# Kernel optimization log

Measured on AMD Instinct MI355X. Metric: run time of the kernel, lower is better.

Reference implementation:

```python
import jax, jax.numpy as jnp
import numpy as np

N = 100000   # nodes
E = 1600000  # directed edges
BN_EPS = 1e-5


def setup_inputs() -> dict:
    key = jax.random.key(0)
    ks = jax.random.split(key, 16)
    x = jax.random.normal(ks[0], (N, 24), dtype=jnp.float32)
    edge_index = jax.random.randint(ks[1], (2, E), 0, N, dtype=jnp.int32)

    def glorot(k, fan_in, fan_out):
        s = jnp.sqrt(6.0 / (fan_in + fan_out)).astype(jnp.float32)
        return jax.random.uniform(k, (fan_in, fan_out), jnp.float32, -s, s)

    return {
        "x": x, "edge_index": edge_index,
        "W1": glorot(ks[2], 24, 128),  "b1": jnp.zeros((128,), jnp.float32),
        "g1": jnp.ones((128,), jnp.float32), "be1": jnp.zeros((128,), jnp.float32),
        "W2": glorot(ks[3], 128, 128), "b2": jnp.zeros((128,), jnp.float32),
        "g2": jnp.ones((128,), jnp.float32), "be2": jnp.zeros((128,), jnp.float32),
        "W3": glorot(ks[4], 128, 64),  "b3": jnp.zeros((64,), jnp.float32),
        "g3": jnp.ones((64,), jnp.float32), "be3": jnp.zeros((64,), jnp.float32),
        "W4": glorot(ks[5], 64, 2),    "b4": jnp.zeros((2,), jnp.float32),
    }


def _gcn_norm(edge_index, n):
    # add self loops, compute D^{-1/2}(A+I)D^{-1/2} edge weights (PyG gcn_norm)
    loop = jnp.arange(n, dtype=edge_index.dtype)
    src = jnp.concatenate([edge_index[0], loop])
    dst = jnp.concatenate([edge_index[1], loop])
    deg = jax.ops.segment_sum(jnp.ones_like(src, dtype=jnp.float32), dst, num_segments=n)
    dinv = jnp.where(deg > 0, jax.lax.rsqrt(deg), 0.0)
    norm = dinv[src] * dinv[dst]  # [E+N]
    return src, dst, norm


def _gcn_conv(x, W, b, src, dst, norm, n):
    h = x @ W                                # [N, F_out] GEMM first (PyG order)
    msg = h[src] * norm[:, None]             # gather + edge scale
    agg = jax.ops.segment_sum(msg, dst, num_segments=n)  # scatter-add
    return agg + b


def _bn(x, gamma, beta):
    # BatchNorm1d, training-mode statistics (biased variance), dropout omitted (eval)
    mean = jnp.mean(x, axis=0)
    var = jnp.var(x, axis=0)
    return (x - mean) * jax.lax.rsqrt(var + BN_EPS) * gamma + beta


def reference(x, edge_index, W1, b1, g1, be1, W2, b2, g2, be2,
              W3, b3, g3, be3, W4, b4):
    n = x.shape[0]
    src, dst, norm = _gcn_norm(edge_index, n)
    h = _bn(jax.nn.relu(_gcn_conv(x, W1, b1, src, dst, norm, n)), g1, be1)
    h = _bn(jax.nn.relu(_gcn_conv(h, W2, b2, src, dst, norm, n)), g2, be2)
    h = _bn(jax.nn.relu(_gcn_conv(h, W3, b3, src, dst, norm, n)), g3, be3)
    out = _gcn_conv(h, W4, b4, src, dst, norm, n)
    return jax.nn.log_softmax(out, axis=1)
```

## Files before the change

### kernel.cpp

```cpp
#include <hip/hip_runtime.h>
#include <hip/hip_fp16.h>

#define BN_EPS 1e-5f

__global__ void k_zero_i(int* __restrict__ p, int n) {
    int i = blockIdx.x * blockDim.x + threadIdx.x;
    if (i < n) p[i] = 0;
}

__global__ void k_count(const int* __restrict__ dst, int* __restrict__ cnt, int E) {
    int e = blockIdx.x * blockDim.x + threadIdx.x;
    if (e < E) atomicAdd(&cnt[dst[e]], 1);
}

__global__ void k_dinv(const int* __restrict__ cnt, float* __restrict__ dinv, int n) {
    int i = blockIdx.x * blockDim.x + threadIdx.x;
    if (i < n) dinv[i] = rsqrtf((float)(cnt[i] + 1));
}

__global__ void k_scan1(const int* __restrict__ cnt, int* __restrict__ rs,
                        int* __restrict__ bsum, int n) {
    __shared__ int sh[1024];
    const int t = threadIdx.x;
    const int gid = blockIdx.x * 1024 + t;
    int v = (gid < n) ? cnt[gid] : 0;
    sh[t] = v;
    __syncthreads();
    for (int off = 1; off < 1024; off <<= 1) {
        int u = (t >= off) ? sh[t - off] : 0;
        __syncthreads();
        sh[t] += u;
        __syncthreads();
    }
    if (gid < n) rs[gid] = sh[t] - v;
    if (t == 1023) bsum[blockIdx.x] = sh[1023];
}

__global__ void k_scan2(int* __restrict__ bsum, int nb) {
    __shared__ int sh[1024];
    const int t = threadIdx.x;
    int v = (t < nb) ? bsum[t] : 0;
    sh[t] = v;
    __syncthreads();
    for (int off = 1; off < 1024; off <<= 1) {
        int u = (t >= off) ? sh[t - off] : 0;
        __syncthreads();
        sh[t] += u;
        __syncthreads();
    }
    if (t < nb) bsum[t] = sh[t] - v;
}

__global__ void k_scan3(int* __restrict__ rs, int* __restrict__ cur,
                        const int* __restrict__ bsum, int n) {
    int i = blockIdx.x * blockDim.x + threadIdx.x;
    if (i < n) {
        int v = rs[i] + bsum[i >> 10];
        rs[i] = v;
        cur[i] = v;
    }
}

__global__ void k_fillx(const int* __restrict__ src, const int* __restrict__ dst,
                        int* __restrict__ cur, int* __restrict__ csrc,
                        int E, int nchunk) {
    const int chunk = blockIdx.x >> 3;
    const int myx = blockIdx.x & 7;
    const int per = (E + nchunk - 1) / nchunk;
    const int lo = chunk * per;
    const int hi = min(lo + per, E);
    for (int e = lo + threadIdx.x; e < hi; e += blockDim.x) {
        int d = dst[e];
        if (((d >> 7) & 7) == myx) {
            int pos = atomicAdd(&cur[d], 1);
            csrc[pos] = src[e];
        }
    }
}

__global__ void k_x2h(const float* __restrict__ x, const float* __restrict__ dinv,
                      __half* __restrict__ xh, int n) {
    int i = blockIdx.x * blockDim.x + threadIdx.x;
    if (i < n * 6) {
        int node = i / 6;
        int j = i - node * 6;
        float dv = dinv[node];
        float4 v = *(const float4*)&x[(size_t)node * 24 + j * 4];
        union { uint2 u; __half2 h[2]; } o;
        o.h[0] = __floats2half2_rn(v.x * dv, v.y * dv);
        o.h[1] = __floats2half2_rn(v.z * dv, v.w * dv);
        *(uint2*)&xh[(size_t)node * 24 + j * 4] = o.u;
    }
}

__global__ void k_agg24h(const __half* __restrict__ xh, const int* __restrict__ rs,
                         const int* __restrict__ rend, const int* __restrict__ csrc,
                         const float* __restrict__ dinv, float* __restrict__ XA, int n) {
    const int g = threadIdx.x >> 3;
    const int j = threadIdx.x & 7;
    const bool act = (j < 6);
    union U { uint2 u; __half2 h[2]; };
    for (int d = blockIdx.x * 32 + g; d < n; d += gridDim.x * 32) {
        const float di = dinv[d];
        const int beg = rs[d], end = rend[d];
        float4 acc = make_float4(0.f, 0.f, 0.f, 0.f);
        if (act) {
            U u; u.u = *(const uint2*)&xh[(size_t)d * 24 + 4 * j];
            float2 f0 = __half22float2(u.h[0]), f1 = __half22float2(u.h[1]);
            acc.x = f0.x; acc.y = f0.y; acc.z = f1.x; acc.w = f1.y;
        }
        int e = beg;
        for (; e + 3 < end; e += 4) {
            int s0 = csrc[e], s1 = csrc[e + 1], s2 = csrc[e + 2], s3 = csrc[e + 3];
            if (act) {
                U u0, u1, u2, u3;
                u0.u = *(const uint2*)&xh[(size_t)s0 * 24 + 4 * j];
                u1.u = *(const uint2*)&xh[(size_t)s1 * 24 + 4 * j];
                u2.u = *(const uint2*)&xh[(size_t)s2 * 24 + 4 * j];
                u3.u = *(const uint2*)&xh[(size_t)s3 * 24 + 4 * j];
                float2 a0 = __half22float2(u0.h[0]), b0 = __half22float2(u0.h[1]);
                float2 a1 = __half22float2(u1.h[0]), b1 = __half22float2(u1.h[1]);
                float2 a2 = __half22float2(u2.h[0]), b2 = __half22float2(u2.h[1]);
                float2 a3 = __half22float2(u3.h[0]), b3 = __half22float2(u3.h[1]);
                acc.x += a0.x + a1.x; acc.y += a0.y + a1.y;
                acc.z += b0.x + b1.x; acc.w += b0.y + b1.y;
                acc.x += a2.x + a3.x; acc.y += a2.y + a3.y;
                acc.z += b2.x + b3.x; acc.w += b2.y + b3.y;
            }
        }
        for (; e < end; ++e) {
            int s = csrc[e];
            if (act) {
                U u; u.u = *(const uint2*)&xh[(size_t)s * 24 + 4 * j];
                float2 f0 = __half22float2(u.h[0]), f1 = __half22float2(u.h[1]);
                acc.x += f0.x; acc.y += f0.y; acc.z += f1.x; acc.w += f1.y;
            }
        }
        if (act) {
            acc.x *= di; acc.y *= di; acc.z *= di; acc.w *= di;
            *(float4*)&XA[(size_t)d * 24 + 4 * j] = acc;
        }
    }
}

template<int K, int F, int RT, bool AFF, bool EPI>
__global__ __launch_bounds__(256) void k_gemm2(const float* __restrict__ X,
        const float* __restrict__ W, const float* __restrict__ aff,
        void* __restrict__ Ov, const float* __restrict__ b,
        float* __restrict__ sums, const float* __restrict__ dinv, int n) {
    constexpr int COLG = F / 4;
    constexpr int ROWG = 256 / COLG;
    constexpr int TR = ROWG * RT;
    __shared__ float sW[K * F];
    __shared__ float sX[TR * K];
    __shared__ float sRed[2 * F];
    const int tid = threadIdx.x;
    const int tx = tid % COLG;
    const int ty = tid / COLG;

    for (int i = tid * 4; i < K * F; i += 1024)
        *(float4*)&sW[i] = *(const float4*)&W[i];

    float4 bv;
    float ls[4], lq[4];
    if constexpr (EPI) {
        bv = *(const float4*)&b[tx * 4];
        #pragma unroll
        for (int c = 0; c < 4; ++c) { ls[c] = 0.f; lq[c] = 0.f; }
    }

    const int ntiles = (n + TR - 1) / TR;
    for (int tile = blockIdx.x; tile < ntiles; tile += gridDim.x) {
        const int r0 = tile * TR;
        __syncthreads();
        for (int i = tid * 4; i < TR * K; i += 1024) {
            const int row = i / K;
            const int kk = i % K;
            float4 v;
            if (r0 + row < n) {
                v = *(const float4*)&X[(size_t)(r0 + row) * K + kk];
                if constexpr (AFF) {
                    v.x = fmaf(v.x, aff[kk],     aff[K + kk]);
                    v.y = fmaf(v.y, aff[kk + 1], aff[K + kk + 1]);
                    v.z = fmaf(v.z, aff[kk + 2], aff[K + kk + 2]);
                    v.w = fmaf(v.w, aff[kk + 3], aff[K + kk + 3]);
                }
            } else {
                v = make_float4(0.f, 0.f, 0.f, 0.f);
            }
            *(float4*)&sX[i] = v;
        }
        __syncthreads();

        float acc[RT][4];
        #pragma unroll
        for (int r = 0; r < RT; ++r)
            #pragma unroll
            for (int c = 0; c < 4; ++c) acc[r][c] = 0.0f;

        for (int k4 = 0; k4 < K; k4 += 4) {
            float xk[RT][4];
            #pragma unroll
            for (int r = 0; r < RT; ++r) {
                float4 t = *(const float4*)&sX[(ty * RT + r) * K + k4];
                xk[r][0] = t.x; xk[r][1] = t.y; xk[r][2] = t.z; xk[r][3] = t.w;
            }
            float4 wv[4];
            #pragma unroll
            for (int kk = 0; kk < 4; ++kk)
                wv[kk] = *(const float4*)&sW[(k4 + kk) * F + tx * 4];
            #pragma unroll
            for (int kk = 0; kk < 4; ++kk)
                #pragma unroll
                for (int r = 0; r < RT; ++r) {
                    const float xr = xk[r][kk];
                    acc[r][0] = fmaf(xr, wv[kk].x, acc[r][0]);
                    acc[r][1] = fmaf(xr, wv[kk].y, acc[r][1]);
                    acc[r][2] = fmaf(xr, wv[kk].z, acc[r][2]);
                    acc[r][3] = fmaf(xr, wv[kk].w, acc[r][3]);
                }
        }

        #pragma unroll
        for (int r = 0; r < RT; ++r) {
            const int row = r0 + ty * RT + r;
            if (row < n) {
                if constexpr (EPI) {
                    float4 o;
                    o.x = fmaxf(acc[r][0] + bv.x, 0.f);
                    o.y = fmaxf(acc[r][1] + bv.y, 0.f);
                    o.z = fmaxf(acc[r][2] + bv.z, 0.f);
                    o.w = fmaxf(acc[r][3] + bv.w, 0.f);
                    ls[0] += o.x; lq[0] += o.x * o.x;
                    ls[1] += o.y; lq[1] += o.y * o.y;
                    ls[2] += o.z; lq[2] += o.z * o.z;
                    ls[3] += o.w; lq[3] += o.w * o.w;
                    *(float4*)&((float*)Ov)[(size_t)row * F + tx * 4] = o;
                } else {
                    const float dv = dinv[row];
                    union { float2 f2; __half2 h2[2]; } u;
                    u.h2[0] = __floats2half2_rn(acc[r][0] * dv, acc[r][1] * dv);
                    u.h2[1] = __floats2half2_rn(acc[r][2] * dv, acc[r][3] * dv);
                    *(float2*)&((__half*)Ov)[(size_t)row * F + tx * 4] = u.f2;
                }
            }
        }
    }

    if constexpr (EPI) {
        __syncthreads();
        if (tid < 2 * F) sRed[tid] = 0.f;
        __syncthreads();
        #pragma unroll
        for (int c = 0; c < 4; ++c) {
            atomicAdd(&sRed[tx * 4 + c], ls[c]);
            atomicAdd(&sRed[F + tx * 4 + c], lq[c]);
        }
        __syncthreads();
        if (tid < F) {
            atomicAdd(&sums[tid], sRed[tid]);
            atomicAdd(&sums[F + tid], sRed[F + tid]);
        }
    }
}

template<int F>
__global__ __launch_bounds__(256) void k_aggh(const __half2* __restrict__ H2,
        const int* __restrict__ rs, const int* __restrict__ rend,
        const int* __restrict__ csrc, const float* __restrict__ dinv,
        const float* __restrict__ b, float* __restrict__ A,
        float* __restrict__ sums, int n) {
    constexpr int LPN = F / 2;
    constexpr int NPW = 64 / LPN;
    __shared__ float sR[2 * F];
    const int tid = threadIdx.x;
    const int lane = tid & 63;
    const int wid = tid >> 6;
    const int sub = lane / LPN;
    const int fl = lane % LPN;
    const float2 bv = make_float2(b[2 * fl], b[2 * fl + 1]);
    const int gw = blockIdx.x * 4 + wid;
    const int nw = gridDim.x * 4;
    float ls0 = 0.f, lq0 = 0.f, ls1 = 0.f, lq1 = 0.f;

    for (int d = gw * NPW + sub; d < n; d += nw * NPW) {
        const int beg = rs[d], end = rend[d];
        const float di = dinv[d];
        float2 h = __half22float2(H2[(size_t)d * LPN + fl]);
        float ax = h.x, ay = h.y;
        int j = beg;
        for (; j + 7 < end; j += 8) {
            int s[8];
            #pragma unroll
            for (int k = 0; k < 8; ++k) s[k] = csrc[j + k];
            __half2 hv[8];
            #pragma unroll
            for (int k = 0; k < 8; ++k) hv[k] = H2[(size_t)s[k] * LPN + fl];
            #pragma unroll
            for (int k = 0; k < 8; ++k) {
                float2 f = __half22float2(hv[k]);
                ax += f.x;
                ay += f.y;
            }
        }
        for (; j + 3 < end; j += 4) {
            int s[4];
            #pragma unroll
            for (int k = 0; k < 4; ++k) s[k] = csrc[j + k];
            __half2 hv[4];
            #pragma unroll
            for (int k = 0; k < 4; ++k) hv[k] = H2[(size_t)s[k] * LPN + fl];
            #pragma unroll
            for (int k = 0; k < 4; ++k) {
                float2 f = __half22float2(hv[k]);
                ax += f.x;
                ay += f.y;
            }
        }
        for (; j < end; ++j) {
            int s = csrc[j];
            float2 f = __half22float2(H2[(size_t)s * LPN + fl]);
            ax += f.x;
            ay += f.y;
        }
        float vx = fmaxf(fmaf(ax, di, bv.x), 0.f);
        float vy = fmaxf(fmaf(ay, di, bv.y), 0.f);
        *(float2*)&A[(size_t)d * F + 2 * fl] = make_float2(vx, vy);
        ls0 += vx; lq0 += vx * vx;
        ls1 += vy; lq1 += vy * vy;
    }

    if (tid < 2 * F) sR[tid] = 0.f;
    __syncthreads();
    atomicAdd(&sR[2 * fl], ls0);
    atomicAdd(&sR[2 * fl + 1], ls1);
    atomicAdd(&sR[F + 2 * fl], lq0);
    atomicAdd(&sR[F + 2 * fl + 1], lq1);
    __syncthreads();
    if (tid < 2 * F) atomicAdd(&sums[tid], sR[tid]);
}

__global__ void k_bnprep(const float* __restrict__ sums, const float* __restrict__ g,
                         const float* __restrict__ be, float* __restrict__ aff,
                         int F, float invn) {
    int f = threadIdx.x;
    if (f < F) {
        float mean = sums[f] * invn;
        float var = sums[F + f] * invn - mean * mean;
        float a = rsqrtf(var + BN_EPS) * g[f];
        aff[f] = a;
        aff[F + f] = be[f] - mean * a;
    }
}

__global__ void k_gemm4(const float* __restrict__ X, const float* __restrict__ W,
                        const float* __restrict__ aff, const float* __restrict__ dinv,
                        float* __restrict__ H, int n) {
    int i = blockIdx.x * blockDim.x + threadIdx.x;
    if (i >= n) return;
    float a0 = 0.0f, a1 = 0.0f;
    #pragma unroll 8
    for (int k = 0; k < 64; ++k) {
        float v = X[i * 64 + k] * aff[k] + aff[64 + k];
        a0 = fmaf(v, W[2 * k], a0);
        a1 = fmaf(v, W[2 * k + 1], a1);
    }
    const float dv = dinv[i];
    H[2 * i] = a0 * dv;
    H[2 * i + 1] = a1 * dv;
}

__global__ void k_last(const float* __restrict__ H, const int* __restrict__ rs,
                       const int* __restrict__ rend, const int* __restrict__ csrc,
                       const float* __restrict__ dinv, const float* __restrict__ b,
                       float* __restrict__ out, int n) {
    int d = blockIdx.x * blockDim.x + threadIdx.x;
    if (d >= n) return;
    const float di = dinv[d];
    float a0 = H[2 * d], a1 = H[2 * d + 1];
    const int beg = rs[d], end = rend[d];
    for (int j = beg; j < end; ++j) {
        int s = csrc[j];
        a0 += H[2 * s];
        a1 += H[2 * s + 1];
    }
    float v0 = fmaf(a0, di, b[0]);
    float v1 = fmaf(a1, di, b[1]);
    float m = fmaxf(v0, v1);
    float l = logf(expf(v0 - m) + expf(v1 - m)) + m;
    out[2 * d] = v0 - l;
    out[2 * d + 1] = v1 - l;
}

extern "C" void kernel_launch(void* const* d_in, const int* in_sizes, int n_in,
                              void* d_out, int out_size, void* d_ws, size_t ws_size,
                              hipStream_t stream) {
    const float* x   = (const float*)d_in[0];
    const int*   ei  = (const int*)d_in[1];
    const float* W1  = (const float*)d_in[2];
    const float* b1  = (const float*)d_in[3];
    const float* g1  = (const float*)d_in[4];
    const float* be1 = (const float*)d_in[5];
    const float* W2  = (const float*)d_in[6];
    const float* b2  = (const float*)d_in[7];
    const float* g2  = (const float*)d_in[8];
    const float* be2 = (const float*)d_in[9];
    const float* W3  = (const float*)d_in[10];
    const float* b3  = (const float*)d_in[11];
    const float* g3  = (const float*)d_in[12];
    const float* be3 = (const float*)d_in[13];
    const float* W4  = (const float*)d_in[14];
    const float* b4  = (const float*)d_in[15];
    float* out = (float*)d_out;

    const int N = in_sizes[0] / 24;
    const int E = in_sizes[1] / 2;
    const int* srcI = ei;
    const int* dstI = ei + E;

    int* cnt   = (int*)d_ws;
    int* rs    = cnt + N;
    int* cur   = rs + N;
    int* csrc  = cur + N;
    int* bsum  = csrc + E;
    float* dinv = (float*)(bsum + 1024);
    float* Hbase = dinv + N;
    float* A    = Hbase + (size_t)N * 128;
    float* S    = A + (size_t)N * 128;
    float* sums1 = S,        *aff1 = S + 256;
    float* sums2 = S + 512,  *aff2 = S + 768;
    float* sums3 = S + 1024, *aff3 = S + 1152;
    float*  XA    = Hbase;
    __half* Hh    = (__half*)Hbase;
    float*  LG    = Hbase;
    __half* xh    = (__half*)A;

    hipMemsetAsync(S, 0, 1280 * sizeof(float), stream);

    const int TB = 256;
    const int nb1024 = (N + 1023) / 1024;

    k_zero_i<<<(N + TB - 1) / TB, TB, 0, stream>>>(cnt, N);
    k_count<<<(E + TB - 1) / TB, TB, 0, stream>>>(dstI, cnt, E);
    k_dinv<<<(N + TB - 1) / TB, TB, 0, stream>>>(cnt, dinv, N);
    k_scan1<<<nb1024, 1024, 0, stream>>>(cnt, rs, bsum, N);
    k_scan2<<<1, 1024, 0, stream>>>(bsum, nb1024);
    k_scan3<<<(N + TB - 1) / TB, TB, 0, stream>>>(rs, cur, bsum, N);
    k_fillx<<<256 * 8, TB, 0, stream>>>(srcI, dstI, cur, csrc, E, 256);

    k_x2h<<<(N * 6 + TB - 1) / TB, TB, 0, stream>>>(x, dinv, xh, N);
    k_agg24h<<<2048, 256, 0, stream>>>(xh, rs, cur, csrc, dinv, XA, N);
    k_gemm2<24, 128, 4, false, true><<<1024, 256, 0, stream>>>(XA, W1, nullptr, A, b1, sums1, nullptr, N);
    k_bnprep<<<1, 128, 0, stream>>>(sums1, g1, be1, aff1, 128, 1.0f / (float)N);

    k_gemm2<128, 128, 4, true, false><<<1024, 256, 0, stream>>>(A, W2, aff1, Hh, nullptr, nullptr, dinv, N);
    k_aggh<128><<<2048, 256, 0, stream>>>((const __half2*)Hh, rs, cur, csrc, dinv, b2, A, sums2, N);
    k_bnprep<<<1, 128, 0, stream>>>(sums2, g2, be2, aff2, 128, 1.0f / (float)N);

    k_gemm2<128, 64, 2, true, false><<<1024, 256, 0, stream>>>(A, W3, aff2, Hh, nullptr, nullptr, dinv, N);
    k_aggh<64><<<2048, 256, 0, stream>>>((const __half2*)Hh, rs, cur, csrc, dinv, b3, A, sums3, N);
    k_bnprep<<<1, 64, 0, stream>>>(sums3, g3, be3, aff3, 64, 1.0f / (float)N);

    k_gemm4<<<(N + TB - 1) / TB, TB, 0, stream>>>(A, W4, aff3, dinv, LG, N);
    k_last<<<(N + TB - 1) / TB, TB, 0, stream>>>(LG, rs, cur, csrc, dinv, b4, out, N);
}
```

Before: 544.5 us.

## Fold BN-prep into consumer GEMMs, fuse dinv into scan, split aggregation kernels

Removes the three single-block k_bnprep launches by computing the BatchNorm affine into shared memory at the start of each consuming GEMM. Folds the dinv computation into k_scan3 and replaces k_zero_i with a memset. The F=64 aggregation now uses a whole wavefront per node, with the two half-waves taking alternate edges and combining through a shuffle. The F=128 aggregation gains a 16-wide unrolled gather. The intent is fewer launches and more memory-level parallelism in the gather, at the cost of every GEMM block recomputing the BN statistics and more registers.

```diff
diff --git a/kernel.cpp b/kernel.cpp
--- a/kernel.cpp
+++ b/kernel.cpp
@@ -2,20 +2,10 @@
 #include <hip/hip_fp16.h>
 
 #define BN_EPS 1e-5f
-
-__global__ void k_zero_i(int* __restrict__ p, int n) {
-    int i = blockIdx.x * blockDim.x + threadIdx.x;
-    if (i < n) p[i] = 0;
-}
 
 __global__ void k_count(const int* __restrict__ dst, int* __restrict__ cnt, int E) {
     int e = blockIdx.x * blockDim.x + threadIdx.x;
     if (e < E) atomicAdd(&cnt[dst[e]], 1);
-}
-
-__global__ void k_dinv(const int* __restrict__ cnt, float* __restrict__ dinv, int n) {
-    int i = blockIdx.x * blockDim.x + threadIdx.x;
-    if (i < n) dinv[i] = rsqrtf((float)(cnt[i] + 1));
 }
 
 __global__ void k_scan1(const int* __restrict__ cnt, int* __restrict__ rs,
@@ -52,12 +42,14 @@
 }
 
 __global__ void k_scan3(int* __restrict__ rs, int* __restrict__ cur,
-                        const int* __restrict__ bsum, int n) {
+                        const int* __restrict__ bsum, const int* __restrict__ cnt,
+                        float* __restrict__ dinv, int n) {
     int i = blockIdx.x * blockDim.x + threadIdx.x;
     if (i < n) {
         int v = rs[i] + bsum[i >> 10];
         rs[i] = v;
         cur[i] = v;
+        dinv[i] = rsqrtf((float)(cnt[i] + 1));
     }
 }
 
@@ -145,18 +137,30 @@
 
 template<int K, int F, int RT, bool AFF, bool EPI>
 __global__ __launch_bounds__(256) void k_gemm2(const float* __restrict__ X,
-        const float* __restrict__ W, const float* __restrict__ aff,
+        const float* __restrict__ W, const float* __restrict__ sums,
+        const float* __restrict__ gv, const float* __restrict__ bev, float invn,
         void* __restrict__ Ov, const float* __restrict__ b,
-        float* __restrict__ sums, const float* __restrict__ dinv, int n) {
+        float* __restrict__ osums, const float* __restrict__ dinv, int n) {
     constexpr int COLG = F / 4;
     constexpr int ROWG = 256 / COLG;
     constexpr int TR = ROWG * RT;
     __shared__ float sW[K * F];
     __shared__ float sX[TR * K];
     __shared__ float sRed[2 * F];
+    __shared__ float sAff[AFF ? 2 * K : 1];
     const int tid = threadIdx.x;
     const int tx = tid % COLG;
     const int ty = tid / COLG;
+
+    if constexpr (AFF) {
+        if (tid < K) {
+            float mean = sums[tid] * invn;
+            float var = sums[K + tid] * invn - mean * mean;
+            float a = rsqrtf(var + BN_EPS) * gv[tid];
+            sAff[tid] = a;
+            sAff[K + tid] = bev[tid] - mean * a;
+        }
+    }
 
     for (int i = tid * 4; i < K * F; i += 1024)
         *(float4*)&sW[i] = *(const float4*)&W[i];
@@ -180,10 +184,10 @@
             if (r0 + row < n) {
                 v = *(const float4*)&X[(size_t)(r0 + row) * K + kk];
                 if constexpr (AFF) {
-                    v.x = fmaf(v.x, aff[kk],     aff[K + kk]);
-                    v.y = fmaf(v.y, aff[kk + 1], aff[K + kk + 1]);
-                    v.z = fmaf(v.z, aff[kk + 2], aff[K + kk + 2]);
-                    v.w = fmaf(v.w, aff[kk + 3], aff[K + kk + 3]);
+                    v.x = fmaf(v.x, sAff[kk],     sAff[K + kk]);
+                    v.y = fmaf(v.y, sAff[kk + 1], sAff[K + kk + 1]);
+                    v.z = fmaf(v.z, sAff[kk + 2], sAff[K + kk + 2]);
+                    v.w = fmaf(v.w, sAff[kk + 3], sAff[K + kk + 3]);
                 }
             } else {
                 v = make_float4(0.f, 0.f, 0.f, 0.f);
@@ -258,49 +262,56 @@
         }
         __syncthreads();
         if (tid < F) {
-            atomicAdd(&sums[tid], sRed[tid]);
-            atomicAdd(&sums[F + tid], sRed[F + tid]);
-        }
-    }
-}
-
-template<int F>
-__global__ __launch_bounds__(256) void k_aggh(const __half2* __restrict__ H2,
+            atomicAdd(&osums[tid], sRed[tid]);
+            atomicAdd(&osums[F + tid], sRed[F + tid]);
+        }
+    }
+}
+
+__global__ __launch_bounds__(256) void k_aggh128(const __half2* __restrict__ H2,
         const int* __restrict__ rs, const int* __restrict__ rend,
         const int* __restrict__ csrc, const float* __restrict__ dinv,
         const float* __restrict__ b, float* __restrict__ A,
         float* __restrict__ sums, int n) {
-    constexpr int LPN = F / 2;
-    constexpr int NPW = 64 / LPN;
-    __shared__ float sR[2 * F];
+    __shared__ float sR[256];
     const int tid = threadIdx.x;
-    const int lane = tid & 63;
+    const int fl = tid & 63;
     const int wid = tid >> 6;
-    const int sub = lane / LPN;
-    const int fl = lane % LPN;
     const float2 bv = make_float2(b[2 * fl], b[2 * fl + 1]);
     const int gw = blockIdx.x * 4 + wid;
     const int nw = gridDim.x * 4;
     float ls0 = 0.f, lq0 = 0.f, ls1 = 0.f, lq1 = 0.f;
 
-    for (int d = gw * NPW + sub; d < n; d += nw * NPW) {
+    for (int d = gw; d < n; d += nw) {
         const int beg = rs[d], end = rend[d];
         const float di = dinv[d];
-        float2 h = __half22float2(H2[(size_t)d * LPN + fl]);
+        float2 h = __half22float2(H2[(size_t)d * 64 + fl]);
         float ax = h.x, ay = h.y;
         int j = beg;
+        for (; j + 15 < end; j += 16) {
+            int s[16];
+            #pragma unroll
+            for (int k = 0; k < 16; ++k) s[k] = csrc[j + k];
+            __half2 hv[16];
+            #pragma unroll
+            for (int k = 0; k < 16; ++k) hv[k] = H2[(size_t)s[k] * 64 + fl];
+            #pragma unroll
+            for (int k = 0; k < 16; ++k) {
+                float2 f = __half22float2(hv[k]);
+                ax += f.x; ay += f.y;
+            }
+        }
         for (; j + 7 < end; j += 8) {
             int s[8];
             #pragma unroll
             for (int k = 0; k < 8; ++k) s[k] = csrc[j + k];
             __half2 hv[8];
             #pragma unroll
-            for (int k = 0; k < 8; ++k) hv[k] = H2[(size_t)s[k] * LPN + fl];
+            for (int k = 0; k < 8; ++k) hv[k] = H2[(size_t)s[k] * 64 + fl];
             #pragma unroll
             for (int k = 0; k < 8; ++k) {
                 float2 f = __half22float2(hv[k]);
-                ax += f.x;
-                ay += f.y;
+                ax += f.x; ay += f.y;
             }
         }
         for (; j + 3 < end; j += 4) {
@@ -309,59 +320,138 @@
             for (int k = 0; k < 4; ++k) s[k] = csrc[j + k];
             __half2 hv[4];
             #pragma unroll
-            for (int k = 0; k < 4; ++k) hv[k] = H2[(size_t)s[k] * LPN + fl];
+            for (int k = 0; k < 4; ++k) hv[k] = H2[(size_t)s[k] * 64 + fl];
             #pragma unroll
             for (int k = 0; k < 4; ++k) {
                 float2 f = __half22float2(hv[k]);
-                ax += f.x;
-                ay += f.y;
+                ax += f.x; ay += f.y;
             }
         }
         for (; j < end; ++j) {
-            int s = csrc[j];
-            float2 f = __half22float2(H2[(size_t)s * LPN + fl]);
-            ax += f.x;
-            ay += f.y;
+            float2 f = __half22float2(H2[(size_t)csrc[j] * 64 + fl]);
+            ax += f.x; ay += f.y;
         }
         float vx = fmaxf(fmaf(ax, di, bv.x), 0.f);
         float vy = fmaxf(fmaf(ay, di, bv.y), 0.f);
-        *(float2*)&A[(size_t)d * F + 2 * fl] = make_float2(vx, vy);
+        *(float2*)&A[(size_t)d * 128 + 2 * fl] = make_float2(vx, vy);
         ls0 += vx; lq0 += vx * vx;
         ls1 += vy; lq1 += vy * vy;
     }
 
-    if (tid < 2 * F) sR[tid] = 0.f;
+    sR[tid] = 0.f;
     __syncthreads();
     atomicAdd(&sR[2 * fl], ls0);
     atomicAdd(&sR[2 * fl + 1], ls1);
-    atomicAdd(&sR[F + 2 * fl], lq0);
-    atomicAdd(&sR[F + 2 * fl + 1], lq1);
-    __syncthreads();
-    if (tid < 2 * F) atomicAdd(&sums[tid], sR[tid]);
-}
-
-__global__ void k_bnprep(const float* __restrict__ sums, const float* __restrict__ g,
-                         const float* __restrict__ be, float* __restrict__ aff,
-                         int F, float invn) {
-    int f = threadIdx.x;
-    if (f < F) {
-        float mean = sums[f] * invn;
-        float var = sums[F + f] * invn - mean * mean;
-        float a = rsqrtf(var + BN_EPS) * g[f];
-        aff[f] = a;
-        aff[F + f] = be[f] - mean * a;
-    }
-}
-
-__global__ void k_gemm4(const float* __restrict__ X, const float* __restrict__ W,
-                        const float* __restrict__ aff, const float* __restrict__ dinv,
-                        float* __restrict__ H, int n) {
-    int i = blockIdx.x * blockDim.x + threadIdx.x;
+    __syncthreads();
+    if (tid < 128) atomicAdd(&sums[tid], sR[tid]);
+    __syncthreads();
+    sR[tid] = 0.f;
+    __syncthreads();
+    atomicAdd(&sR[2 * fl], lq0);
+    atomicAdd(&sR[2 * fl + 1], lq1);
+    __syncthreads();
+    if (tid < 128) atomicAdd(&sums[128 + tid], sR[tid]);
+}
+
+__global__ __launch_bounds__(256) void k_aggh64(const __half2* __restrict__ H2,
+        const int* __restrict__ rs, const int* __restrict__ rend,
+        const int* __restrict__ csrc, const float* __restrict__ dinv,
+        const float* __restrict__ b, float* __restrict__ A,
+        float* __restrict__ sums, int n) {
+    __shared__ float sR[128];
+    const int tid = threadIdx.x;
+    const int lane = tid & 63;
+    const int wid = tid >> 6;
+    const int fl = lane & 31;
+    const int half = lane >> 5;
+    const float2 bv = make_float2(b[2 * fl], b[2 * fl + 1]);
+    const int gw = blockIdx.x * 4 + wid;
+    const int nw = gridDim.x * 4;
+    float ls0 = 0.f, lq0 = 0.f, ls1 = 0.f, lq1 = 0.f;
+
+    for (int d = gw; d < n; d += nw) {
+        const int beg = rs[d], end = rend[d];
+        const float di = dinv[d];
+        float ax = 0.f, ay = 0.f;
+        if (half == 0) {
+            float2 h = __half22float2(H2[(size_t)d * 32 + fl]);
+            ax = h.x; ay = h.y;
+        }
+        int j = beg + half;
+        for (; j + 14 < end; j += 16) {
+            int s[8];
+            #pragma unroll
+            for (int k = 0; k < 8; ++k) s[k] = csrc[j + 2 * k];
+            __half2 hv[8];
+            #pragma unroll
+            for (int k = 0; k < 8; ++k) hv[k] = H2[(size_t)s[k] * 32 + fl];
+            #pragma unroll
+            for (int k = 0; k < 8; ++k) {
+                float2 f = __half22float2(hv[k]);
+                ax += f.x; ay += f.y;
+            }
+        }
+        for (; j + 6 < end; j += 8) {
+            int s[4];
+            #pragma unroll
+            for (int k = 0; k < 4; ++k) s[k] = csrc[j + 2 * k];
+            __half2 hv[4];
+            #pragma unroll
+            for (int k = 0; k < 4; ++k) hv[k] = H2[(size_t)s[k] * 32 + fl];
+            #pragma unroll
+            for (int k = 0; k < 4; ++k) {
+                float2 f = __half22float2(hv[k]);
+                ax += f.x; ay += f.y;
+            }
+        }
+        for (; j < end; j += 2) {
+            float2 f = __half22float2(H2[(size_t)csrc[j] * 32 + fl]);
+            ax += f.x; ay += f.y;
+        }
+        ax += __shfl_xor(ax, 32);
+        ay += __shfl_xor(ay, 32);
+        if (half == 0) {
+            float vx = fmaxf(fmaf(ax, di, bv.x), 0.f);
+            float vy = fmaxf(fmaf(ay, di, bv.y), 0.f);
+            *(float2*)&A[(size_t)d * 64 + 2 * fl] = make_float2(vx, vy);
+            ls0 += vx; lq0 += vx * vx;
+            ls1 += vy; lq1 += vy * vy;
+        }
+    }
+
+    if (tid < 128) sR[tid] = 0.f;
+    __syncthreads();
+    if ((lane >> 5) == 0) {
+        atomicAdd(&sR[2 * fl], ls0);
+        atomicAdd(&sR[2 * fl + 1], ls1);
+        atomicAdd(&sR[64 + 2 * fl], lq0);
+        atomicAdd(&sR[64 + 2 * fl + 1], lq1);
+    }
+    __syncthreads();
+    if (tid < 64) atomicAdd(&sums[tid], sR[tid]);
+    else if (tid < 128) atomicAdd(&sums[64 + tid - 64], sR[tid]);
+}
+
+__global__ __launch_bounds__(256) void k_gemm4(const float* __restrict__ X,
+        const float* __restrict__ W, const float* __restrict__ sums,
+        const float* __restrict__ gv, const float* __restrict__ bev, float invn,
+        const float* __restrict__ dinv, float* __restrict__ H, int n) {
+    __shared__ float sAff[128];
+    const int tid = threadIdx.x;
+    if (tid < 64) {
+        float mean = sums[tid] * invn;
+        float var = sums[64 + tid] * invn - mean * mean;
+        float a = rsqrtf(var + BN_EPS) * gv[tid];
+        sAff[tid] = a;
+        sAff[64 + tid] = bev[tid] - mean * a;
+    }
+    __syncthreads();
+    int i = blockIdx.x * blockDim.x + tid;
     if (i >= n) return;
     float a0 = 0.0f, a1 = 0.0f;
     #pragma unroll 8
     for (int k = 0; k < 64; ++k) {
-        float v = X[i * 64 + k] * aff[k] + aff[64 + k];
+        float v = fmaf(X[(size_t)i * 64 + k], sAff[k], sAff[64 + k]);
         a0 = fmaf(v, W[2 * k], a0);
         a1 = fmaf(v, W[2 * k + 1], a1);
     }
@@ -417,6 +507,7 @@
     const int E = in_sizes[1] / 2;
     const int* srcI = ei;
     const int* dstI = ei + E;
+    const float invn = 1.0f / (float)N;
 
     int* cnt   = (int*)d_ws;
     int* rs    = cnt + N;
@@ -427,40 +518,39 @@
     float* Hbase = dinv + N;
     float* A    = Hbase + (size_t)N * 128;
     float* S    = A + (size_t)N * 128;
-    float* sums1 = S,        *aff1 = S + 256;
-    float* sums2 = S + 512,  *aff2 = S + 768;
-    float* sums3 = S + 1024, *aff3 = S + 1152;
+    float* sums1 = S;
+    float* sums2 = S + 256;
+    float* sums3 = S + 512;
     float*  XA    = Hbase;
     __half* Hh    = (__half*)Hbase;
     float*  LG    = Hbase;
     __half* xh    = (__half*)A;
 
-    hipMemsetAsync(S, 0, 1280 * sizeof(float), stream);
+    hipMemsetAsync(S, 0, 640 * sizeof(float), stream);
+    hipMemsetAsync(cnt, 0, (size_t)N * sizeof(int), stream);
 
     const int TB = 256;
     const int nb1024 = (N + 1023) / 1024;
 
-    k_zero_i<<<(N + TB - 1) / TB, TB, 0, stream>>>(cnt, N);
     k_count<<<(E + TB - 1) / TB, TB, 0, stream>>>(dstI, cnt, E);
-    k_dinv<<<(N + TB - 1) / TB, TB, 0, stream>>>(cnt, dinv, N);
     k_scan1<<<nb1024, 1024, 0, stream>>>(cnt, rs, bsum, N);
     k_scan2<<<1, 1024, 0, stream>>>(bsum, nb1024);
-    k_scan3<<<(N + TB - 1) / TB, TB, 0, stream>>>(rs, cur, bsum, N);
+    k_scan3<<<(N + TB - 1) / TB, TB, 0, stream>>>(rs, cur, bsum, cnt, dinv, N);
     k_fillx<<<256 * 8, TB, 0, stream>>>(srcI, dstI, cur, csrc, E, 256);
 
     k_x2h<<<(N * 6 + TB - 1) / TB, TB, 0, stream>>>(x, dinv, xh, N);
     k_agg24h<<<2048, 256, 0, stream>>>(xh, rs, cur, csrc, dinv, XA, N);
-    k_gemm2<24, 128, 4, false, true><<<1024, 256, 0, stream>>>(XA, W1, nullptr, A, b1, sums1, nullptr, N);
-    k_bnprep<<<1, 128, 0, stream>>>(sums1, g1, be1, aff1, 128, 1.0f / (float)N);
-
-    k_gemm2<128, 128, 4, true, false><<<1024, 256, 0, stream>>>(A, W2, aff1, Hh, nullptr, nullptr, dinv, N);
-    k_aggh<128><<<2048, 256, 0, stream>>>((const __half2*)Hh, rs, cur, csrc, dinv, b2, A, sums2, N);
-    k_bnprep<<<1, 128, 0, stream>>>(sums2, g2, be2, aff2, 128, 1.0f / (float)N);
-
-    k_gemm2<128, 64, 2, true, false><<<1024, 256, 0, stream>>>(A, W3, aff2, Hh, nullptr, nullptr, dinv, N);
-    k_aggh<64><<<2048, 256, 0, stream>>>((const __half2*)Hh, rs, cur, csrc, dinv, b3, A, sums3, N);
-    k_bnprep<<<1, 64, 0, stream>>>(sums3, g3, be3, aff3, 64, 1.0f / (float)N);
-
-    k_gemm4<<<(N + TB - 1) / TB, TB, 0, stream>>>(A, W4, aff3, dinv, LG, N);
+    k_gemm2<24, 128, 4, false, true><<<1024, 256, 0, stream>>>(
+        XA, W1, nullptr, nullptr, nullptr, 0.f, A, b1, sums1, nullptr, N);
+
+    k_gemm2<128, 128, 4, true, false><<<1024, 256, 0, stream>>>(
+        A, W2, sums1, g1, be1, invn, Hh, nullptr, nullptr, dinv, N);
+    k_aggh128<<<2048, 256, 0, stream>>>((const __half2*)Hh, rs, cur, csrc, dinv, b2, A, sums2, N);
+
+    k_gemm2<128, 64, 2, true, false><<<1024, 256, 0, stream>>>(
+        A, W3, sums2, g2, be2, invn, Hh, nullptr, nullptr, dinv, N);
+    k_aggh64<<<2048, 256, 0, stream>>>((const __half2*)Hh, rs, cur, csrc, dinv, b3, A, sums3, N);
+
+    k_gemm4<<<(N + TB - 1) / TB, TB, 0, stream>>>(A, W4, sums3, g3, be3, invn, dinv, LG, N);
     k_last<<<(N + TB - 1) / TB, TB, 0, stream>>>(LG, rs, cur, csrc, dinv, b4, out, N);
 }
```

Result: slower. 586.4 us (+7.7%).

## Fuse BN-prep into GEMMs, dinv into scan, and partition degree counting

Applied to the files above, without the earlier changes.

Removes the three single-block k_bnprep launches by computing the BatchNorm affine coefficients into shared memory at the start of each consuming GEMM block. Folds the dinv computation into k_scan3 and replaces k_zero_i with a memset. Switches the degree-count kernel to the same chunked, destination-bucketed scheme as the fill kernel to localize atomics. This cuts launch count and serialized tiny kernels, but every GEMM block now redundantly recomputes the affine terms and the count kernel reads dst eight times.

```diff
diff --git a/kernel.cpp b/kernel.cpp
--- a/kernel.cpp
+++ b/kernel.cpp
@@ -3,19 +3,17 @@
 
 #define BN_EPS 1e-5f
 
-__global__ void k_zero_i(int* __restrict__ p, int n) {
-    int i = blockIdx.x * blockDim.x + threadIdx.x;
-    if (i < n) p[i] = 0;
-}
-
-__global__ void k_count(const int* __restrict__ dst, int* __restrict__ cnt, int E) {
-    int e = blockIdx.x * blockDim.x + threadIdx.x;
-    if (e < E) atomicAdd(&cnt[dst[e]], 1);
-}
-
-__global__ void k_dinv(const int* __restrict__ cnt, float* __restrict__ dinv, int n) {
-    int i = blockIdx.x * blockDim.x + threadIdx.x;
-    if (i < n) dinv[i] = rsqrtf((float)(cnt[i] + 1));
+__global__ void k_countx(const int* __restrict__ dst, int* __restrict__ cnt,
+                         int E, int nchunk) {
+    const int chunk = blockIdx.x >> 3;
+    const int myx = blockIdx.x & 7;
+    const int per = (E + nchunk - 1) / nchunk;
+    const int lo = chunk * per;
+    const int hi = min(lo + per, E);
+    for (int e = lo + threadIdx.x; e < hi; e += blockDim.x) {
+        int d = dst[e];
+        if (((d >> 7) & 7) == myx) atomicAdd(&cnt[d], 1);
+    }
 }
 
 __global__ void k_scan1(const int* __restrict__ cnt, int* __restrict__ rs,
@@ -52,12 +50,14 @@
 }
 
 __global__ void k_scan3(int* __restrict__ rs, int* __restrict__ cur,
-                        const int* __restrict__ bsum, int n) {
+                        const int* __restrict__ bsum, const int* __restrict__ cnt,
+                        float* __restrict__ dinv, int n) {
     int i = blockIdx.x * blockDim.x + threadIdx.x;
     if (i < n) {
         int v = rs[i] + bsum[i >> 10];
         rs[i] = v;
         cur[i] = v;
+        dinv[i] = rsqrtf((float)(cnt[i] + 1));
     }
 }
 
@@ -145,18 +145,30 @@
 
 template<int K, int F, int RT, bool AFF, bool EPI>
 __global__ __launch_bounds__(256) void k_gemm2(const float* __restrict__ X,
-        const float* __restrict__ W, const float* __restrict__ aff,
+        const float* __restrict__ W, const float* __restrict__ sums,
+        const float* __restrict__ gv, const float* __restrict__ bev, float invn,
         void* __restrict__ Ov, const float* __restrict__ b,
-        float* __restrict__ sums, const float* __restrict__ dinv, int n) {
+        float* __restrict__ osums, const float* __restrict__ dinv, int n) {
     constexpr int COLG = F / 4;
     constexpr int ROWG = 256 / COLG;
     constexpr int TR = ROWG * RT;
     __shared__ float sW[K * F];
     __shared__ float sX[TR * K];
     __shared__ float sRed[2 * F];
+    __shared__ float sAff[AFF ? 2 * K : 1];
     const int tid = threadIdx.x;
     const int tx = tid % COLG;
     const int ty = tid / COLG;
+
+    if constexpr (AFF) {
+        if (tid < K) {
+            float mean = sums[tid] * invn;
+            float var = sums[K + tid] * invn - mean * mean;
+            float a = rsqrtf(var + BN_EPS) * gv[tid];
+            sAff[tid] = a;
+            sAff[K + tid] = bev[tid] - mean * a;
+        }
+    }
 
     for (int i = tid * 4; i < K * F; i += 1024)
         *(float4*)&sW[i] = *(const float4*)&W[i];
@@ -180,10 +192,10 @@
             if (r0 + row < n) {
                 v = *(const float4*)&X[(size_t)(r0 + row) * K + kk];
                 if constexpr (AFF) {
-                    v.x = fmaf(v.x, aff[kk],     aff[K + kk]);
-                    v.y = fmaf(v.y, aff[kk + 1], aff[K + kk + 1]);
-                    v.z = fmaf(v.z, aff[kk + 2], aff[K + kk + 2]);
-                    v.w = fmaf(v.w, aff[kk + 3], aff[K + kk + 3]);
+                    v.x = fmaf(v.x, sAff[kk],     sAff[K + kk]);
+                    v.y = fmaf(v.y, sAff[kk + 1], sAff[K + kk + 1]);
+                    v.z = fmaf(v.z, sAff[kk + 2], sAff[K + kk + 2]);
+                    v.w = fmaf(v.w, sAff[kk + 3], sAff[K + kk + 3]);
                 }
             } else {
                 v = make_float4(0.f, 0.f, 0.f, 0.f);
@@ -258,8 +270,8 @@
         }
         __syncthreads();
         if (tid < F) {
-            atomicAdd(&sums[tid], sRed[tid]);
-            atomicAdd(&sums[F + tid], sRed[F + tid]);
+            atomicAdd(&osums[tid], sRed[tid]);
+            atomicAdd(&osums[F + tid], sRed[F + tid]);
         }
     }
 }
@@ -340,28 +352,26 @@
     if (tid < 2 * F) atomicAdd(&sums[tid], sR[tid]);
 }
 
-__global__ void k_bnprep(const float* __restrict__ sums, const float* __restrict__ g,
-                         const float* __restrict__ be, float* __restrict__ aff,
-                         int F, float invn) {
-    int f = threadIdx.x;
-    if (f < F) {
-        float mean = sums[f] * invn;
-        float var = sums[F + f] * invn - mean * mean;
-        float a = rsqrtf(var + BN_EPS) * g[f];
-        aff[f] = a;
-        aff[F + f] = be[f] - mean * a;
-    }
-}
-
-__global__ void k_gemm4(const float* __restrict__ X, const float* __restrict__ W,
-                        const float* __restrict__ aff, const float* __restrict__ dinv,
-                        float* __restrict__ H, int n) {
-    int i = blockIdx.x * blockDim.x + threadIdx.x;
+__global__ __launch_bounds__(256) void k_gemm4(const float* __restrict__ X,
+        const float* __restrict__ W, const float* __restrict__ sums,
+        const float* __restrict__ gv, const float* __restrict__ bev, float invn,
+        const float* __restrict__ dinv, float* __restrict__ H, int n) {
+    __shared__ float sAff[128];
+    const int tid = threadIdx.x;
+    if (tid < 64) {
+        float mean = sums[tid] * invn;
+        float var = sums[64 + tid] * invn - mean * mean;
+        float a = rsqrtf(var + BN_EPS) * gv[tid];
+        sAff[tid] = a;
+        sAff[64 + tid] = bev[tid] - mean * a;
+    }
+    __syncthreads();
+    int i = blockIdx.x * blockDim.x + tid;
     if (i >= n) return;
     float a0 = 0.0f, a1 = 0.0f;
     #pragma unroll 8
     for (int k = 0; k < 64; ++k) {
-        float v = X[i * 64 + k] * aff[k] + aff[64 + k];
+        float v = fmaf(X[(size_t)i * 64 + k], sAff[k], sAff[64 + k]);
         a0 = fmaf(v, W[2 * k], a0);
         a1 = fmaf(v, W[2 * k + 1], a1);
     }
@@ -417,6 +427,7 @@
     const int E = in_sizes[1] / 2;
     const int* srcI = ei;
     const int* dstI = ei + E;
+    const float invn = 1.0f / (float)N;
 
     int* cnt   = (int*)d_ws;
     int* rs    = cnt + N;
@@ -427,40 +438,39 @@
     float* Hbase = dinv + N;
     float* A    = Hbase + (size_t)N * 128;
     float* S    = A + (size_t)N * 128;
-    float* sums1 = S,        *aff1 = S + 256;
-    float* sums2 = S + 512,  *aff2 = S + 768;
-    float* sums3 = S + 1024, *aff3 = S + 1152;
+    float* sums1 = S;
+    float* sums2 = S + 256;
+    float* sums3 = S + 512;
     float*  XA    = Hbase;
     __half* Hh    = (__half*)Hbase;
     float*  LG    = Hbase;
     __half* xh    = (__half*)A;
 
-    hipMemsetAsync(S, 0, 1280 * sizeof(float), stream);
+    hipMemsetAsync(S, 0, 640 * sizeof(float), stream);
+    hipMemsetAsync(cnt, 0, (size_t)N * sizeof(int), stream);
 
     const int TB = 256;
     const int nb1024 = (N + 1023) / 1024;
 
-    k_zero_i<<<(N + TB - 1) / TB, TB, 0, stream>>>(cnt, N);
-    k_count<<<(E + TB - 1) / TB, TB, 0, stream>>>(dstI, cnt, E);
-    k_dinv<<<(N + TB - 1) / TB, TB, 0, stream>>>(cnt, dinv, N);
+    k_countx<<<256 * 8, TB, 0, stream>>>(dstI, cnt, E, 256);
     k_scan1<<<nb1024, 1024, 0, stream>>>(cnt, rs, bsum, N);
     k_scan2<<<1, 1024, 0, stream>>>(bsum, nb1024);
-    k_scan3<<<(N + TB - 1) / TB, TB, 0, stream>>>(rs, cur, bsum, N);
+    k_scan3<<<(N + TB - 1) / TB, TB, 0, stream>>>(rs, cur, bsum, cnt, dinv, N);
     k_fillx<<<256 * 8, TB, 0, stream>>>(srcI, dstI, cur, csrc, E, 256);
 
     k_x2h<<<(N * 6 + TB - 1) / TB, TB, 0, stream>>>(x, dinv, xh, N);
     k_agg24h<<<2048, 256, 0, stream>>>(xh, rs, cur, csrc, dinv, XA, N);
-    k_gemm2<24, 128, 4, false, true><<<1024, 256, 0, stream>>>(XA, W1, nullptr, A, b1, sums1, nullptr, N);
-    k_bnprep<<<1, 128, 0, stream>>>(sums1, g1, be1, aff1, 128, 1.0f / (float)N);
-
-    k_gemm2<128, 128, 4, true, false><<<1024, 256, 0, stream>>>(A, W2, aff1, Hh, nullptr, nullptr, dinv, N);
+    k_gemm2<24, 128, 4, false, true><<<1024, 256, 0, stream>>>(
+        XA, W1, nullptr, nullptr, nullptr, 0.f, A, b1, sums1, nullptr, N);
+
+    k_gemm2<128, 128, 4, true, false><<<1024, 256, 0, stream>>>(
+        A, W2, sums1, g1, be1, invn, Hh, nullptr, nullptr, dinv, N);
     k_aggh<128><<<2048, 256, 0, stream>>>((const __half2*)Hh, rs, cur, csrc, dinv, b2, A, sums2, N);
-    k_bnprep<<<1, 128, 0, stream>>>(sums2, g2, be2, aff2, 128, 1.0f / (float)N);
-
-    k_gemm2<128, 64, 2, true, false><<<1024, 256, 0, stream>>>(A, W3, aff2, Hh, nullptr, nullptr, dinv, N);
+
+    k_gemm2<128, 64, 2, true, false><<<1024, 256, 0, stream>>>(
+        A, W3, sums2, g2, be2, invn, Hh, nullptr, nullptr, dinv, N);
     k_aggh<64><<<2048, 256, 0, stream>>>((const __half2*)Hh, rs, cur, csrc, dinv, b3, A, sums3, N);
-    k_bnprep<<<1, 64, 0, stream>>>(sums3, g3, be3, aff3, 64, 1.0f / (float)N);
-
-    k_gemm4<<<(N + TB - 1) / TB, TB, 0, stream>>>(A, W4, aff3, dinv, LG, N);
+
+    k_gemm4<<<(N + TB - 1) / TB, TB, 0, stream>>>(A, W4, sums3, g3, be3, invn, dinv, LG, N);
     k_last<<<(N + TB - 1) / TB, TB, 0, stream>>>(LG, rs, cur, csrc, dinv, b4, out, N);
 }
```

New measurement: 577.2 us. +6.0%, slower.
